# Optimization experiments

Measured on AMD Instinct MI355X. Metric: run time of the kernel, lower is better.

Reference implementation:

```python
import jax, jax.numpy as jnp
import numpy as np

LN_EPS = 1e-5
H_STEP = 0.1


def _mm(W, x):
    # conv1d with kernel size 1 == channel matmul: [O,C] x [B,C,N] -> [B,O,N]
    return jnp.einsum('oc,bcn->bon', W, x)


def _layer_norm_all(x):
    # F.layer_norm(x, x.shape): normalize over the ENTIRE tensor, no affine
    m = jnp.mean(x)
    v = jnp.mean((x - m) ** 2)
    return (x - m) * jax.lax.rsqrt(v + LN_EPS)


def double_layer(x, K1, K2):
    # dropout omitted (eval mode / deterministic reference)
    x = _mm(K1, x)
    x = _layer_norm_all(x)
    x = jax.nn.relu(x)
    return _mm(K2, x)


def setup_inputs() -> dict:
    key = jax.random.key(0)
    ks = jax.random.split(key, 16)
    B, XIN, EIN, HID, OUT, NL = 1, 32, 32, 128, 64, 4
    N, E = 50000, 500000
    stdv = 0.001
    inp = {
        'xn': jax.random.normal(ks[0], (B, XIN, N), dtype=jnp.float32),
        'xe': jax.random.normal(ks[1], (B, EIN, E), dtype=jnp.float32),
        'iInd': jax.random.randint(ks[2], (E,), 0, N),
        'jInd': jax.random.randint(ks[3], (E,), 0, N),
        'K1Nopen': jax.random.normal(ks[4], (HID, XIN), dtype=jnp.float32) * stdv,
        'K2Nopen': jax.random.normal(ks[5], (HID, HID), dtype=jnp.float32) * stdv,
        'K1Eopen': jax.random.normal(ks[6], (HID, EIN), dtype=jnp.float32) * stdv,
        'K2Eopen': jax.random.normal(ks[7], (HID, HID), dtype=jnp.float32) * stdv,
        'KNout': jax.random.normal(ks[8], (OUT, HID), dtype=jnp.float32) * stdv,
        'KE1': jax.random.normal(ks[9], (NL, 2 * HID, 3 * HID), dtype=jnp.float32) * stdv,
        'KE2': jax.random.normal(ks[10], (NL, HID, 2 * HID), dtype=jnp.float32) * stdv,
        'KN1': jax.random.normal(ks[11], (NL, 2 * HID, 3 * HID), dtype=jnp.float32) * stdv,
        'KN2': jax.random.normal(ks[12], (NL, HID, 2 * HID), dtype=jnp.float32) * stdv,
    }
    return inp


def reference(xn, xe, iInd, jInd, K1Nopen, K2Nopen, K1Eopen, K2Eopen, KNout,
              KE1, KE2, KN1, KN2):
    xn = double_layer(xn, K1Nopen, K2Nopen)
    xe = double_layer(xe, K1Eopen, K2Eopen)
    N = xn.shape[2]
    # Source sets row = col = Graph.iInd (faithful replication)
    row = iInd
    col = iInd
    nlayers = KE1.shape[0]
    for i in range(nlayers):
        # gather node feats to edges, concat with edge feats: [B, 3*hid, E]
        xec = jnp.concatenate([xn[:, :, row], xn[:, :, col], xe], axis=1)
        xec = double_layer(xec, KE1[i], KE2[i])
        # scatter edge feats back to both endpoints
        zeros = jnp.zeros((xec.shape[0], xec.shape[1], N), dtype=xec.dtype)
        s_i = zeros.at[:, :, iInd].add(xec)
        s_j = zeros.at[:, :, jInd].add(xec)
        ave = 0.5 * (s_i + s_j)          # edgeAve(method='ave')
        div = s_i - s_j                   # edgeDiv
        xnc = jnp.concatenate([ave, div, xn], axis=1)
        xnc = double_layer(xnc, KN1[i], KN2[i])
        xn = xn + H_STEP * xnc
        xe = xe + H_STEP * xec
    xn = _mm(KNout, xn)
    return xn, xe
```

## Files before the change

kernel.cpp:

```cpp
#include <hip/hip_runtime.h>
#include <hip/hip_bf16.h>


typedef __hip_bfloat16 bf16;
typedef __attribute__((ext_vector_type(8))) short bf16x8;
typedef __attribute__((ext_vector_type(4))) float f32x4;

#define HSTEP 0.1f

__device__ __forceinline__ bf16  f2b(float v){ return __float2bfloat16(v); }
__device__ __forceinline__ unsigned int f2bu(float v){
    return (unsigned int)__builtin_bit_cast(unsigned short, __float2bfloat16(v));
}
__device__ __forceinline__ void store8(float* p, const float* a){
    *(float4*)p       = make_float4(a[0],a[1],a[2],a[3]);
    *((float4*)p + 1) = make_float4(a[4],a[5],a[6],a[7]);
}

__device__ __forceinline__ uint4 lnrelu_pack(uint4 r, float mean, float rstd){
    float f0 = __uint_as_float(r.x << 16), f1 = __uint_as_float(r.x & 0xffff0000u);
    float f2 = __uint_as_float(r.y << 16), f3 = __uint_as_float(r.y & 0xffff0000u);
    float f4 = __uint_as_float(r.z << 16), f5 = __uint_as_float(r.z & 0xffff0000u);
    float f6 = __uint_as_float(r.w << 16), f7 = __uint_as_float(r.w & 0xffff0000u);
    f0 = fmaxf(0.f,(f0-mean)*rstd); f1 = fmaxf(0.f,(f1-mean)*rstd);
    f2 = fmaxf(0.f,(f2-mean)*rstd); f3 = fmaxf(0.f,(f3-mean)*rstd);
    f4 = fmaxf(0.f,(f4-mean)*rstd); f5 = fmaxf(0.f,(f5-mean)*rstd);
    f6 = fmaxf(0.f,(f6-mean)*rstd); f7 = fmaxf(0.f,(f7-mean)*rstd);
    uint4 q;
    q.x = f2bu(f0) | (f2bu(f1) << 16);
    q.y = f2bu(f2) | (f2bu(f3) << 16);
    q.z = f2bu(f4) | (f2bu(f5) << 16);
    q.w = f2bu(f6) | (f2bu(f7) << 16);
    return q;
}
__device__ __forceinline__ uint4 pack8f(float4 a, float4 b){
    uint4 q;
    q.x = f2bu(a.x) | (f2bu(a.y) << 16);
    q.y = f2bu(a.z) | (f2bu(a.w) << 16);
    q.z = f2bu(b.x) | (f2bu(b.y) << 16);
    q.w = f2bu(b.z) | (f2bu(b.w) << 16);
    return q;
}

__device__ __forceinline__ void block_red2(double ls, double ls2, double* sredw,
                                           int tx, double* redp, int bid)
{
    #pragma unroll
    for (int off = 32; off; off >>= 1) {
        ls  += __shfl_down(ls,  off, 64);
        ls2 += __shfl_down(ls2, off, 64);
    }
    const int w = tx >> 6, l = tx & 63;
    if (l == 0) { sredw[2*w] = ls; sredw[2*w+1] = ls2; }
    __syncthreads();
    if (tx == 0) {
        redp[2*(size_t)bid]     = ((sredw[0]+sredw[2])+(sredw[4]+sredw[6]));
        redp[2*(size_t)bid + 1] = ((sredw[1]+sredw[3])+(sredw[5]+sredw[7]));
    }
}

__global__ void wt_transpose(const float* __restrict__ src, float* __restrict__ dst,
                             int O, int C) {
    int i = blockIdx.x*256 + threadIdx.x;
    if (i >= O*C) return;
    int o = i / C, c = i - o*C;
    dst[c*O + o] = src[i];
}

__global__ void wt_ke1_bf(const float* __restrict__ src, bf16* __restrict__ dst) {
    int i = blockIdx.x*256 + threadIdx.x;
    if (i >= 256*256) return;
    int o = i >> 8, c = i & 255;
    float v;
    if (c < 128) v = src[o*384 + c] + src[o*384 + 128 + c];
    else         v = src[o*384 + 128 + c];
    dst[i] = f2b(v);
}

__global__ void wt_cast_bf(const float* __restrict__ src, bf16* __restrict__ dst, int cnt) {
    int i = blockIdx.x*256 + threadIdx.x;
    if (i < cnt) dst[i] = f2b(src[i]);
}

__global__ void csr_hist(const int* __restrict__ ind, int* __restrict__ cnt, int E){
    int e = blockIdx.x*256 + threadIdx.x;
    if (e < E) atomicAdd(&cnt[ind[e]], 1);
}

__global__ void csr_scan(const int* __restrict__ cnt, int* __restrict__ rowptr,
                         int* __restrict__ cursor, int Nn)
{
    __shared__ int part[256];
    int tx = threadIdx.x;
    int chunk = (Nn + 255) / 256;
    int a0 = tx * chunk;
    int a1 = a0 + chunk; if (a1 > Nn) a1 = Nn; if (a0 > Nn) a0 = Nn;
    int s = 0;
    for (int i = a0; i < a1; ++i) s += cnt[i];
    part[tx] = s;
    __syncthreads();
    for (int d = 1; d < 256; d <<= 1) {
        int v = (tx >= d) ? part[tx - d] : 0;
        __syncthreads();
        part[tx] += v;
        __syncthreads();
    }
    int run = (tx == 0) ? 0 : part[tx - 1];
    for (int i = a0; i < a1; ++i) {
        rowptr[i] = run; cursor[i] = run;
        run += cnt[i];
    }
    if (tx == 255) rowptr[Nn] = run;
}

__global__ void csr_fill(const int* __restrict__ ind, int* __restrict__ cursor,
                         int* __restrict__ eadj, int E){
    int e = blockIdx.x*256 + threadIdx.x;
    if (e < E) {
        int p = atomicAdd(&cursor[ind[e]], 1);
        eadj[p] = e;
    }
}

__launch_bounds__(256)
__global__ void gather_nodes(const bf16* __restrict__ y,
                             const int* __restrict__ rowptr,
                             const int* __restrict__ eadj,
                             float* __restrict__ s, int Nn)
{
    int wid  = threadIdx.x >> 6;
    int lane = threadIdx.x & 63;
    int node = blockIdx.x * 4 + wid;
    if (node >= Nn) return;
    int k0 = rowptr[node], k1 = rowptr[node+1];
    const unsigned* yu = (const unsigned*)y;
    float a0=0.f,a1=0.f,b0=0.f,b1=0.f,c0=0.f,c1=0.f,d0=0.f,d1=0.f;
    int k = k0;
    for (; k + 4 <= k1; k += 4) {
        int e0 = eadj[k], e1 = eadj[k+1], e2 = eadj[k+2], e3 = eadj[k+3];
        unsigned v0 = yu[(size_t)e0*64 + lane];
        unsigned v1 = yu[(size_t)e1*64 + lane];
        unsigned v2 = yu[(size_t)e2*64 + lane];
        unsigned v3 = yu[(size_t)e3*64 + lane];
        a0 += __uint_as_float(v0 << 16); a1 += __uint_as_float(v0 & 0xffff0000u);
        b0 += __uint_as_float(v1 << 16); b1 += __uint_as_float(v1 & 0xffff0000u);
        c0 += __uint_as_float(v2 << 16); c1 += __uint_as_float(v2 & 0xffff0000u);
        d0 += __uint_as_float(v3 << 16); d1 += __uint_as_float(v3 & 0xffff0000u);
    }
    for (; k < k1; ++k) {
        unsigned v = yu[(size_t)eadj[k]*64 + lane];
        a0 += __uint_as_float(v << 16); a1 += __uint_as_float(v & 0xffff0000u);
    }
    a0 += (b0 + c0) + d0;
    a1 += (b1 + c1) + d1;
    *(float2*)(s + (size_t)node*128 + lane*2) = make_float2(a0, a1);
}

__global__ void ln_reduce(const double* __restrict__ redp, int nb,
                          float* __restrict__ ln, double cnt)
{
    __shared__ double s0[256], s1[256];
    int tx = threadIdx.x;
    double a = 0.0, b = 0.0;
    for (int i = tx; i < nb; i += 256) { a += redp[2*i]; b += redp[2*i+1]; }
    s0[tx] = a; s1[tx] = b;
    __syncthreads();
    for (int s = 128; s > 0; s >>= 1) {
        if (tx < s) { s0[tx] += s0[tx+s]; s1[tx] += s1[tx+s]; }
        __syncthreads();
    }
    if (tx == 0) {
        double m = s0[0] / cnt;
        double var = s1[0] / cnt - m*m;
        if (var < 0.0) var = 0.0;
        ln[0] = (float)m;
        ln[1] = (float)(1.0 / sqrt(var + 1e-5));
    }
}

__launch_bounds__(256)
__global__ void mfma_mm1_edge(const bf16* __restrict__ Wb,
                              const bf16* __restrict__ xnb,
                              const float* __restrict__ xe,
                              const int* __restrict__ iInd,
                              bf16* __restrict__ ucm,
                              int E, double* __restrict__ redp)
{
    __shared__ __align__(16) unsigned short Vs[64*256];
    __shared__ double sredw[8];
    const int tx = threadIdx.x;
    const int x0 = blockIdx.x * 64;
    const int e = tx >> 2, q4 = tx & 3;
    const int xedge = x0 + e;
    const bool ev = xedge < E;
    const int gidx = ev ? iInd[xedge] : 0;
    const unsigned swz = (unsigned)((e & 7) << 3);

    #pragma unroll
    for (int p = 0; p < 4; ++p) {
        int k0 = q4*8 + p*32;
        uint4 v = make_uint4(0,0,0,0);
        if (ev) v = *(const uint4*)(xnb + (size_t)gidx*128 + k0);
        *(uint4*)&Vs[(unsigned)(e*256 + k0) ^ swz] = v;
    }
    #pragma unroll
    for (int p = 0; p < 4; ++p) {
        int k0 = q4*8 + p*32;
        uint4 v = make_uint4(0,0,0,0);
        if (ev) {
            const float* s = xe + (size_t)xedge*128 + k0;
            v = pack8f(*(const float4*)s, *(const float4*)(s + 4));
        }
        *(uint4*)&Vs[(unsigned)(e*256 + 128 + k0) ^ swz] = v;
    }
    __syncthreads();

    const int w = tx >> 6, l = tx & 63;
    const int colb = l & 15, grp = l >> 4;
    f32x4 acc[4][4];
    #pragma unroll
    for (int m=0;m<4;++m)
        #pragma unroll
        for (int n=0;n<4;++n) acc[m][n] = (f32x4){0.f,0.f,0.f,0.f};

    const bf16* wp = Wb + (size_t)(w*64 + colb)*256 + grp*8;
    bf16x8 aC[4], aN[4];
    #pragma unroll
    for (int m=0;m<4;++m)
        aC[m] = __builtin_bit_cast(bf16x8, *(const uint4*)(wp + m*16*256));

    #pragma unroll
    for (int kc = 0; kc < 8; ++kc) {
        const int kf = kc*32 + grp*8;
        if (kc < 7) {
            #pragma unroll
            for (int m=0;m<4;++m)
                aN[m] = __builtin_bit_cast(bf16x8,
                          *(const uint4*)(wp + m*16*256 + (kc+1)*32));
        }
        bf16x8 b[4];
        #pragma unroll
        for (int n=0;n<4;++n) {
            int ee = n*16 + colb;
            b[n] = __builtin_bit_cast(bf16x8,
                     *(const uint4*)&Vs[(unsigned)(ee*256 + kf) ^ (unsigned)((ee&7)<<3)]);
        }
        #pragma unroll
        for (int m=0;m<4;++m)
            #pragma unroll
            for (int n=0;n<4;++n)
                acc[m][n] = __builtin_amdgcn_mfma_f32_16x16x32_bf16(aC[m], b[n], acc[m][n], 0, 0, 0);
        #pragma unroll
        for (int m=0;m<4;++m) aC[m] = aN[m];
    }

    double ls = 0.0, ls2 = 0.0;
    #pragma unroll
    for (int n=0;n<4;++n) {
        int edge = x0 + n*16 + colb;
        if (edge < E) {
            #pragma unroll
            for (int m=0;m<4;++m) {
                f32x4 v = acc[m][n];
                ls  += (double)v[0] + (double)v[1] + (double)v[2] + (double)v[3];
                ls2 += (double)v[0]*v[0] + (double)v[1]*v[1]
                     + (double)v[2]*v[2] + (double)v[3]*v[3];
            }
        }
    }

    __syncthreads();
    const int rq = grp*4;
    #pragma unroll
    for (int n=0;n<4;++n) {
        int ee = n*16 + colb;
        #pragma unroll
        for (int m=0;m<4;++m) {
            f32x4 v = acc[m][n];
            int r0 = w*64 + m*16 + rq;
            uint2 q;
            q.x = f2bu(v[0]) | (f2bu(v[1]) << 16);
            q.y = f2bu(v[2]) | (f2bu(v[3]) << 16);
            *(uint2*)&Vs[(unsigned)(ee*256 + r0) ^ (unsigned)((ee&7)<<3)] = q;
        }
    }
    __syncthreads();
    if (ev) {
        #pragma unroll
        for (int p = 0; p < 8; ++p) {
            int c0 = q4*8 + p*32;
            uint4 v = *(uint4*)&Vs[(unsigned)(e*256 + c0) ^ swz];
            *(uint4*)(ucm + (size_t)xedge*256 + c0) = v;
        }
    }
    block_red2(ls, ls2, sredw, tx, redp, blockIdx.x);
}

__launch_bounds__(256)
__global__ void mfma_mm1_node(const bf16* __restrict__ Wb,
                              const float* __restrict__ si,
                              const float* __restrict__ sj,
                              const float* __restrict__ xn,
                              bf16* __restrict__ ucm,
                              int Nn, double* __restrict__ redp)
{
    __shared__ __align__(16) unsigned short Vs[64*384];
    __shared__ double sredw[8];
    const int tx = threadIdx.x;
    const int x0 = blockIdx.x * 64;
    const int e = tx >> 2, q4 = tx & 3;
    const int node = x0 + e;
    const bool nv = node < Nn;
    const unsigned swz = (unsigned)((e & 7) << 3);

    #pragma unroll
    for (int p = 0; p < 4; ++p) {
        int k0 = q4*8 + p*32;
        uint4 va = make_uint4(0,0,0,0), vd = va;
        if (nv) {
            const float* ps = si + (size_t)node*128 + k0;
            const float* pt = sj + (size_t)node*128 + k0;
            float4 a0 = *(const float4*)ps, a1 = *(const float4*)(ps+4);
            float4 b0 = *(const float4*)pt, b1 = *(const float4*)(pt+4);
            float4 av0 = make_float4(0.5f*(a0.x+b0.x),0.5f*(a0.y+b0.y),
                                     0.5f*(a0.z+b0.z),0.5f*(a0.w+b0.w));
            float4 av1 = make_float4(0.5f*(a1.x+b1.x),0.5f*(a1.y+b1.y),
                                     0.5f*(a1.z+b1.z),0.5f*(a1.w+b1.w));
            float4 dv0 = make_float4(a0.x-b0.x,a0.y-b0.y,a0.z-b0.z,a0.w-b0.w);
            float4 dv1 = make_float4(a1.x-b1.x,a1.y-b1.y,a1.z-b1.z,a1.w-b1.w);
            va = pack8f(av0, av1);
            vd = pack8f(dv0, dv1);
        }
        *(uint4*)&Vs[(unsigned)(e*384 + k0) ^ swz] = va;
        *(uint4*)&Vs[(unsigned)(e*384 + 128 + k0) ^ swz] = vd;
    }
    #pragma unroll
    for (int p = 0; p < 4; ++p) {
        int k0 = q4*8 + p*32;
        uint4 v = make_uint4(0,0,0,0);
        if (nv) {
            const float* s = xn + (size_t)node*128 + k0;
            v = pack8f(*(const float4*)s, *(const float4*)(s + 4));
        }
        *(uint4*)&Vs[(unsigned)(e*384 + 256 + k0) ^ swz] = v;
    }
    __syncthreads();

    const int w = tx >> 6, l = tx & 63;
    const int colb = l & 15, grp = l >> 4;
    f32x4 acc[4][4];
    #pragma unroll
    for (int m=0;m<4;++m)
        #pragma unroll
        for (int n=0;n<4;++n) acc[m][n] = (f32x4){0.f,0.f,0.f,0.f};

    const bf16* wp = Wb + (size_t)(w*64 + colb)*384 + grp*8;
    bf16x8 aC[4], aN[4];
    #pragma unroll
    for (int m=0;m<4;++m)
        aC[m] = __builtin_bit_cast(bf16x8, *(const uint4*)(wp + m*16*384));

    #pragma unroll
    for (int kc = 0; kc < 12; ++kc) {
        const int kf = kc*32 + grp*8;
        if (kc < 11) {
            #pragma unroll
            for (int m=0;m<4;++m)
                aN[m] = __builtin_bit_cast(bf16x8,
                          *(const uint4*)(wp + m*16*384 + (kc+1)*32));
        }
        bf16x8 b[4];
        #pragma unroll
        for (int n=0;n<4;++n) {
            int ee = n*16 + colb;
            b[n] = __builtin_bit_cast(bf16x8,
                     *(const uint4*)&Vs[(unsigned)(ee*384 + kf) ^ (unsigned)((ee&7)<<3)]);
        }
        #pragma unroll
        for (int m=0;m<4;++m)
            #pragma unroll
            for (int n=0;n<4;++n)
                acc[m][n] = __builtin_amdgcn_mfma_f32_16x16x32_bf16(aC[m], b[n], acc[m][n], 0, 0, 0);
        #pragma unroll
        for (int m=0;m<4;++m) aC[m] = aN[m];
    }

    double ls = 0.0, ls2 = 0.0;
    const int rq = grp*4;
    #pragma unroll
    for (int n=0;n<4;++n) {
        int nd = x0 + n*16 + colb;
        if (nd < Nn) {
            #pragma unroll
            for (int m=0;m<4;++m) {
                f32x4 v = acc[m][n];
                int r0 = w*64 + m*16 + rq;
                uint2 q;
                q.x = f2bu(v[0]) | (f2bu(v[1]) << 16);
                q.y = f2bu(v[2]) | (f2bu(v[3]) << 16);
                *(uint2*)(ucm + (size_t)nd*256 + r0) = q;
                ls  += (double)v[0] + (double)v[1] + (double)v[2] + (double)v[3];
                ls2 += (double)v[0]*v[0] + (double)v[1]*v[1]
                     + (double)v[2]*v[2] + (double)v[3]*v[3];
            }
        }
    }
    block_red2(ls, ls2, sredw, tx, redp, blockIdx.x);
}

enum { E2_EDGE = 0, E2_NODE = 1, E2_XE0 = 2, E2_XN0 = 3 };

template<int IC, int EPI>
__launch_bounds__(256)
__global__ void mfma_mm2(const bf16* __restrict__ Wb2,
                         const bf16* __restrict__ ucm,
                         const float* __restrict__ ln,
                         float* __restrict__ dst,
                         bf16* __restrict__ yv,
                         bf16* __restrict__ xnb,
                         int n)
{
    __shared__ __align__(16) unsigned short Vs[64*IC];
    const int tx = threadIdx.x;
    const int x0 = blockIdx.x * 64;
    const int e = tx >> 2, q4 = tx & 3;
    const int row = x0 + e;
    const bool rv = row < n;
    const float mean = ln[0], rstd = ln[1];
    const unsigned swz = (unsigned)((e & 7) << 3);

    #pragma unroll
    for (int p = 0; p < IC/32; ++p) {
        int k0 = q4*8 + p*32;
        uint4 v = make_uint4(0,0,0,0);
        if (rv) {
            uint4 r = *(const uint4*)(ucm + (size_t)row*IC + k0);
            v = lnrelu_pack(r, mean, rstd);
        }
        *(uint4*)&Vs[(unsigned)(e*IC + k0) ^ swz] = v;
    }
    __syncthreads();

    const int w = tx >> 6, l = tx & 63;
    const int colb = l & 15, grp = l >> 4;
    f32x4 acc[2][4];
    #pragma unroll
    for (int m=0;m<2;++m)
        #pragma unroll
        for (int nn=0;nn<4;++nn) acc[m][nn] = (f32x4){0.f,0.f,0.f,0.f};

    const bf16* wp = Wb2 + (size_t)(w*32 + colb)*IC + grp*8;
    bf16x8 aC[2], aN[2];
    #pragma unroll
    for (int m=0;m<2;++m)
        aC[m] = __builtin_bit_cast(bf16x8, *(const uint4*)(wp + m*16*IC));

    #pragma unroll
    for (int kc = 0; kc < IC/32; ++kc) {
        const int kf = kc*32 + grp*8;
        if (kc < IC/32 - 1) {
            #pragma unroll
            for (int m=0;m<2;++m)
                aN[m] = __builtin_bit_cast(bf16x8,
                          *(const uint4*)(wp + m*16*IC + (kc+1)*32));
        }
        bf16x8 b[4];
        #pragma unroll
        for (int nn=0;nn<4;++nn) {
            int ee = nn*16 + colb;
            b[nn] = __builtin_bit_cast(bf16x8,
                     *(const uint4*)&Vs[(unsigned)(ee*IC + kf) ^ (unsigned)((ee&7)<<3)]);
        }
        #pragma unroll
        for (int m=0;m<2;++m)
            #pragma unroll
            for (int nn=0;nn<4;++nn)
                acc[m][nn] = __builtin_amdgcn_mfma_f32_16x16x32_bf16(aC[m], b[nn], acc[m][nn], 0, 0, 0);
        #pragma unroll
        for (int m=0;m<2;++m) aC[m] = aN[m];
    }

    const int rq = grp*4;
    #pragma unroll
    for (int nn=0;nn<4;++nn) {
        int x = x0 + nn*16 + colb;
        if (x < n) {
            #pragma unroll
            for (int m=0;m<2;++m) {
                f32x4 v = acc[m][nn];
                int r0 = w*32 + m*16 + rq;
                if constexpr (EPI == E2_EDGE) {
                    uint2 q;
                    q.x = f2bu(v[0]) | (f2bu(v[1]) << 16);
                    q.y = f2bu(v[2]) | (f2bu(v[3]) << 16);
                    *(uint2*)(yv + (size_t)x*128 + r0) = q;
                    float* px = dst + (size_t)x*128 + r0;
                    float4 o = *(float4*)px;
                    o.x += HSTEP*v[0]; o.y += HSTEP*v[1];
                    o.z += HSTEP*v[2]; o.w += HSTEP*v[3];
                    *(float4*)px = o;
                } else if constexpr (EPI == E2_XE0) {
                    *(float4*)(dst + (size_t)x*128 + r0) =
                        make_float4(v[0], v[1], v[2], v[3]);
                } else if constexpr (EPI == E2_NODE) {
                    float* px = dst + (size_t)x*128 + r0;
                    float4 o = *(float4*)px;
                    o.x += HSTEP*v[0]; o.y += HSTEP*v[1];
                    o.z += HSTEP*v[2]; o.w += HSTEP*v[3];
                    *(float4*)px = o;
                    uint2 q;
                    q.x = f2bu(o.x) | (f2bu(o.y) << 16);
                    q.y = f2bu(o.z) | (f2bu(o.w) << 16);
                    *(uint2*)(xnb + (size_t)x*128 + r0) = q;
                } else {
                    *(float4*)(dst + (size_t)x*128 + r0) =
                        make_float4(v[0], v[1], v[2], v[3]);
                    uint2 q;
                    q.x = f2bu(v[0]) | (f2bu(v[1]) << 16);
                    q.y = f2bu(v[2]) | (f2bu(v[3]) << 16);
                    *(uint2*)(xnb + (size_t)x*128 + r0) = q;
                }
            }
        }
    }
}

__launch_bounds__(256)
__global__ void mm1_open(const float* __restrict__ Wt,
                         const float* __restrict__ xin,
                         bf16* __restrict__ ucm,
                         int n, double* __restrict__ redp)
{
    __shared__ float lv[32][64];
    __shared__ double sredw[8];
    const int tx = threadIdx.x;
    const int tr = tx & 31, tc = tx >> 5;
    const int x0 = blockIdx.x * 64;

    float acc[4][8];
    #pragma unroll
    for (int ri=0; ri<4; ++ri)
        #pragma unroll
        for (int ei=0; ei<8; ++ei) acc[ri][ei] = 0.f;

    #pragma unroll
    for (int k=0; k<2; ++k) {
        int id = k*256 + tx;
        int xq = id & 15, cc = id >> 4;
        int x = x0 + xq*4;
        const float* p = xin + (size_t)cc*n + x;
        float4 q;
        if (x + 3 < n) q = *(const float4*)p;
        else {
            q.x = (x  <n)?p[0]:0.f; q.y = (x+1<n)?p[1]:0.f;
            q.z = (x+2<n)?p[2]:0.f; q.w = (x+3<n)?p[3]:0.f;
        }
        *(float4*)&lv[cc][xq*4] = q;
    }
    __syncthreads();
    for (int cc=0; cc<32; ++cc) {
        const float* wrow = Wt + cc*128 + tr*4;
        float w[4] = {wrow[0], wrow[1], wrow[2], wrow[3]};
        float vv[8];
        #pragma unroll
        for (int ei=0; ei<8; ++ei) vv[ei] = lv[cc][tc*8+ei];
        #pragma unroll
        for (int ri=0; ri<4; ++ri)
            #pragma unroll
            for (int ei=0; ei<8; ++ei)
                acc[ri][ei] = fmaf(w[ri], vv[ei], acc[ri][ei]);
    }

    double ls = 0.0, ls2 = 0.0;
    #pragma unroll
    for (int ei=0; ei<8; ++ei) {
        int x = x0 + tc*8 + ei;
        if (x < n) {
            uint2 bq;
            bq.x = f2bu(acc[0][ei]) | (f2bu(acc[1][ei]) << 16);
            bq.y = f2bu(acc[2][ei]) | (f2bu(acc[3][ei]) << 16);
            *(uint2*)(ucm + (size_t)x*128 + tr*4) = bq;
            #pragma unroll
            for (int ri=0; ri<4; ++ri) {
                double y = acc[ri][ei]; ls += y; ls2 += y*y;
            }
        }
    }
    block_red2(ls, ls2, sredw, tx, redp, blockIdx.x);
}

__launch_bounds__(256)
__global__ void final_out(const float* __restrict__ Wt,
                          const float* __restrict__ xncm,
                          float* __restrict__ out, int n)
{
    __shared__ float lv[32][64];
    const int tx = threadIdx.x;
    const int tr = tx & 31, tc = tx >> 5;
    const int x0 = blockIdx.x * 64;

    float acc[2][8];
    #pragma unroll
    for (int ri=0; ri<2; ++ri)
        #pragma unroll
        for (int ei=0; ei<8; ++ei) acc[ri][ei] = 0.f;

    for (int c0 = 0; c0 < 128; c0 += 32) {
        #pragma unroll
        for (int k=0; k<2; ++k) {
            int id = k*256 + tx;
            int xx = id & 63, cg = id >> 6;
            int x = x0 + xx;
            float4 q;
            if (x < n) q = *(const float4*)(xncm + (size_t)x*128 + c0 + cg*4);
            else { q.x=q.y=q.z=q.w=0.f; }
            lv[cg*4+0][xx]=q.x; lv[cg*4+1][xx]=q.y;
            lv[cg*4+2][xx]=q.z; lv[cg*4+3][xx]=q.w;
        }
        __syncthreads();
        for (int cc=0; cc<32; ++cc) {
            const float* wrow = Wt + (c0+cc)*64 + tr*2;
            float w0 = wrow[0], w1 = wrow[1];
            float vv[8];
            #pragma unroll
            for (int ei=0; ei<8; ++ei) vv[ei] = lv[cc][tc*8+ei];
            #pragma unroll
            for (int ei=0; ei<8; ++ei) {
                acc[0][ei] = fmaf(w0, vv[ei], acc[0][ei]);
                acc[1][ei] = fmaf(w1, vv[ei], acc[1][ei]);
            }
        }
        __syncthreads();
    }

    const bool full = (x0 + 64 <= n);
    #pragma unroll
    for (int ri=0; ri<2; ++ri) {
        int r = tr*2 + ri;
        if (full) {
            store8(out + (size_t)r*n + x0 + tc*8, acc[ri]);
        } else {
            #pragma unroll
            for (int ei=0; ei<8; ++ei) {
                int x = x0 + tc*8 + ei;
                if (x < n) out[(size_t)r*n + x] = acc[ri][ei];
            }
        }
    }
}

__launch_bounds__(256)
__global__ void xe_transpose(const float* __restrict__ xe, float* __restrict__ out, int E)
{
    __shared__ float T[128][65];
    const int tx = threadIdx.x;
    const int x0 = blockIdx.x * 64;
    const int es = tx & 63, cg = tx >> 6;
    #pragma unroll
    for (int p = 0; p < 8; ++p) {
        int c = cg*4 + p*16;
        if (x0 + es < E) {
            float4 v = *(const float4*)(xe + (size_t)(x0+es)*128 + c);
            T[c+0][es] = v.x; T[c+1][es] = v.y; T[c+2][es] = v.z; T[c+3][es] = v.w;
        }
    }
    __syncthreads();
    const int c2 = tx >> 1, eo = (tx & 1)*32;
    if (x0 + 64 <= E) {
        #pragma unroll
        for (int q = 0; q < 8; ++q) {
            float4 v = make_float4(T[c2][eo+q*4], T[c2][eo+q*4+1],
                                   T[c2][eo+q*4+2], T[c2][eo+q*4+3]);
            *(float4*)(out + (size_t)c2*E + x0 + eo + q*4) = v;
        }
    } else {
        for (int q = 0; q < 32; ++q) {
            int x = x0 + eo + q;
            if (x < E) out[(size_t)c2*E + x] = T[c2][eo+q];
        }
    }
}

extern "C" void kernel_launch(void* const* d_in, const int* in_sizes, int n_in,
                              void* d_out, int out_size, void* d_ws, size_t ws_size,
                              hipStream_t stream)
{
    const int N = in_sizes[0] / 32;
    const int E = in_sizes[1] / 32;
    const int NL = in_sizes[9] / (256*384);

    const float* xn_in = (const float*)d_in[0];
    const float* xe_in = (const float*)d_in[1];
    const int*   iInd  = (const int*)d_in[2];
    const int*   jInd  = (const int*)d_in[3];
    const float* K1N = (const float*)d_in[4];
    const float* K2N = (const float*)d_in[5];
    const float* K1E = (const float*)d_in[6];
    const float* K2E = (const float*)d_in[7];
    const float* KNo = (const float*)d_in[8];
    const float* KE1 = (const float*)d_in[9];
    const float* KE2 = (const float*)d_in[10];
    const float* KN1 = (const float*)d_in[11];
    const float* KN2 = (const float*)d_in[12];

    char* base = (char*)d_ws;
    size_t off = 0;
    auto carve = [&](size_t bytes)->void* {
        void* p = base + off; off += (bytes + 255) & ~(size_t)255; return p;
    };
    float* xn  = (float*)carve((size_t)128*N*sizeof(float));
    float* xe  = (float*)carve((size_t)128*E*sizeof(float));
    bf16*  u   = (bf16*) carve((size_t)256*E*sizeof(bf16));
    bf16*  y   = (bf16*) carve((size_t)128*E*sizeof(bf16));
    float* si  = (float*)carve((size_t)128*N*sizeof(float));
    float* sj  = (float*)carve((size_t)128*N*sizeof(float));
    float* wtsf= (float*)carve((32*128*2 + 128*64)*sizeof(float));
    bf16*  Wb   = (bf16*)carve((size_t)256*256*sizeof(bf16));
    bf16*  Wb2  = (bf16*)carve((size_t)128*256*sizeof(bf16));
    bf16*  Wn1b = (bf16*)carve((size_t)256*384*sizeof(bf16));
    bf16*  Wn2b = (bf16*)carve((size_t)128*256*sizeof(bf16));
    bf16*  K2Nb = (bf16*)carve((size_t)128*128*sizeof(bf16));
    bf16*  K2Eb = (bf16*)carve((size_t)128*128*sizeof(bf16));
    bf16*  xnb  = (bf16*)carve((size_t)128*N*sizeof(bf16));
    double* redp = (double*)carve(2*8192*sizeof(double));
    float* lnp = (float*)carve(256);
    int* cnt      = (int*)carve((size_t)N*sizeof(int));
    int* rowptr_i = (int*)carve((size_t)(N+1)*sizeof(int));
    int* rowptr_j = (int*)carve((size_t)(N+1)*sizeof(int));
    int* cur_i    = (int*)carve((size_t)N*sizeof(int));
    int* cur_j    = (int*)carve((size_t)N*sizeof(int));
    int* eadj_i   = (int*)carve((size_t)E*sizeof(int));
    int* eadj_j   = (int*)carve((size_t)E*sizeof(int));

    if (ws_size < off) return;

    float* K1Nt = wtsf;
    float* K1Et = K1Nt + 32*128;
    float* KNoT = K1Et + 32*128;

    wt_transpose<<<dim3((128*32 +255)/256),dim3(256),0,stream>>>(K1N, K1Nt, 128, 32);
    wt_transpose<<<dim3((128*32 +255)/256),dim3(256),0,stream>>>(K1E, K1Et, 128, 32);
    wt_transpose<<<dim3((64*128 +255)/256),dim3(256),0,stream>>>(KNo, KNoT, 64, 128);
    wt_cast_bf<<<dim3(64),dim3(256),0,stream>>>(K2N, K2Nb, 128*128);
    wt_cast_bf<<<dim3(64),dim3(256),0,stream>>>(K2E, K2Eb, 128*128);

    const int gN = (N + 63)/64, gE = (E + 63)/64;
    const int gEb = (E + 255)/256;

    (void)hipMemsetAsync(cnt, 0, (size_t)N*sizeof(int), stream);
    csr_hist<<<gEb,256,0,stream>>>(iInd, cnt, E);
    csr_scan<<<1,256,0,stream>>>(cnt, rowptr_i, cur_i, N);
    csr_fill<<<gEb,256,0,stream>>>(iInd, cur_i, eadj_i, E);
    (void)hipMemsetAsync(cnt, 0, (size_t)N*sizeof(int), stream);
    csr_hist<<<gEb,256,0,stream>>>(jInd, cnt, E);
    csr_scan<<<1,256,0,stream>>>(cnt, rowptr_j, cur_j, N);
    csr_fill<<<gEb,256,0,stream>>>(jInd, cur_j, eadj_j, E);

    mm1_open<<<gN,256,0,stream>>>(K1Nt, xn_in, u, N, redp);
    ln_reduce<<<1,256,0,stream>>>(redp, gN, lnp, 128.0*N);
    mfma_mm2<128,E2_XN0><<<gN,256,0,stream>>>(K2Nb, u, lnp, xn, nullptr, xnb, N);

    mm1_open<<<gE,256,0,stream>>>(K1Et, xe_in, u, E, redp);
    ln_reduce<<<1,256,0,stream>>>(redp, gE, lnp, 128.0*E);
    mfma_mm2<128,E2_XE0><<<gE,256,0,stream>>>(K2Eb, u, lnp, xe, nullptr, nullptr, E);

    for (int l = 0; l < NL; ++l) {
        wt_ke1_bf<<<dim3(256),dim3(256),0,stream>>>(KE1 + (size_t)l*256*384, Wb);
        wt_cast_bf<<<dim3(128),dim3(256),0,stream>>>(KE2 + (size_t)l*128*256, Wb2, 128*256);
        wt_cast_bf<<<dim3(384),dim3(256),0,stream>>>(KN1 + (size_t)l*256*384, Wn1b, 256*384);
        wt_cast_bf<<<dim3(128),dim3(256),0,stream>>>(KN2 + (size_t)l*128*256, Wn2b, 128*256);

        mfma_mm1_edge<<<gE,256,0,stream>>>(Wb, xnb, xe, iInd, u, E, redp);
        ln_reduce<<<1,256,0,stream>>>(redp, gE, lnp, 256.0*E);
        mfma_mm2<256,E2_EDGE><<<gE,256,0,stream>>>(Wb2, u, lnp, xe, y, nullptr, E);
        gather_nodes<<<(N+3)/4,256,0,stream>>>(y, rowptr_i, eadj_i, si, N);
        gather_nodes<<<(N+3)/4,256,0,stream>>>(y, rowptr_j, eadj_j, sj, N);

        mfma_mm1_node<<<gN,256,0,stream>>>(Wn1b, si, sj, xn, u, N, redp);
        ln_reduce<<<1,256,0,stream>>>(redp, gN, lnp, 256.0*N);
        mfma_mm2<256,E2_NODE><<<gN,256,0,stream>>>(Wn2b, u, lnp, xn, nullptr, xnb, N);
    }

    final_out<<<gN,256,0,stream>>>(KNoT, xn, (float*)d_out, N);
    xe_transpose<<<gE,256,0,stream>>>(xe, (float*)d_out + (size_t)64*N, E);
}
```

Before: 3.659 ms.

## Persistent grid-stride MFMA kernels with register prefetch and bf16 edge-feature shadow

The edge mm1 and mm2 kernels become persistent, capped at 2048 blocks, and loop over 64-column tiles. Each iteration prefetches the next tile's inputs into registers while the current tile is computed. The mm2 epilogue now also writes a bf16 shadow copy of xe, so the edge mm1 reads bf16 instead of fp32 and packing on the fly. mm1_edge drops its LDS transpose and writes its output directly. The weight-fragment double buffering is replaced with plain per-k loads, which trades register pressure against exposed load latency, and the extra shadow store adds write traffic.

```diff
diff --git a/kernel.cpp b/kernel.cpp
--- a/kernel.cpp
+++ b/kernel.cpp
@@ -181,116 +181,97 @@
 __launch_bounds__(256)
 __global__ void mfma_mm1_edge(const bf16* __restrict__ Wb,
                               const bf16* __restrict__ xnb,
-                              const float* __restrict__ xe,
+                              const bf16* __restrict__ xeb,
                               const int* __restrict__ iInd,
                               bf16* __restrict__ ucm,
-                              int E, double* __restrict__ redp)
+                              int E, int ntiles, double* __restrict__ redp)
 {
     __shared__ __align__(16) unsigned short Vs[64*256];
     __shared__ double sredw[8];
     const int tx = threadIdx.x;
-    const int x0 = blockIdx.x * 64;
     const int e = tx >> 2, q4 = tx & 3;
-    const int xedge = x0 + e;
-    const bool ev = xedge < E;
-    const int gidx = ev ? iInd[xedge] : 0;
     const unsigned swz = (unsigned)((e & 7) << 3);
-
-    #pragma unroll
-    for (int p = 0; p < 4; ++p) {
-        int k0 = q4*8 + p*32;
-        uint4 v = make_uint4(0,0,0,0);
-        if (ev) v = *(const uint4*)(xnb + (size_t)gidx*128 + k0);
-        *(uint4*)&Vs[(unsigned)(e*256 + k0) ^ swz] = v;
-    }
-    #pragma unroll
-    for (int p = 0; p < 4; ++p) {
-        int k0 = q4*8 + p*32;
-        uint4 v = make_uint4(0,0,0,0);
-        if (ev) {
-            const float* s = xe + (size_t)xedge*128 + k0;
-            v = pack8f(*(const float4*)s, *(const float4*)(s + 4));
-        }
-        *(uint4*)&Vs[(unsigned)(e*256 + 128 + k0) ^ swz] = v;
-    }
-    __syncthreads();
-
     const int w = tx >> 6, l = tx & 63;
     const int colb = l & 15, grp = l >> 4;
-    f32x4 acc[4][4];
-    #pragma unroll
-    for (int m=0;m<4;++m)
-        #pragma unroll
-        for (int n=0;n<4;++n) acc[m][n] = (f32x4){0.f,0.f,0.f,0.f};
-
-    const bf16* wp = Wb + (size_t)(w*64 + colb)*256 + grp*8;
-    bf16x8 aC[4], aN[4];
-    #pragma unroll
-    for (int m=0;m<4;++m)
-        aC[m] = __builtin_bit_cast(bf16x8, *(const uint4*)(wp + m*16*256));
-
-    #pragma unroll
-    for (int kc = 0; kc < 8; ++kc) {
-        const int kf = kc*32 + grp*8;
-        if (kc < 7) {
+
+    uint4 rN[4] = {{0,0,0,0},{0,0,0,0},{0,0,0,0},{0,0,0,0}};
+    uint4 rE[4] = {{0,0,0,0},{0,0,0,0},{0,0,0,0},{0,0,0,0}};
+
+    auto issue = [&](int tt){
+        int xedge = tt*64 + e;
+        if (xedge < E) {
+            int gidx = iInd[xedge];
+            #pragma unroll
+            for (int p=0;p<4;++p)
+                rN[p] = *(const uint4*)(xnb + (size_t)gidx*128 + q4*8 + p*32);
+            #pragma unroll
+            for (int p=0;p<4;++p)
+                rE[p] = *(const uint4*)(xeb + (size_t)xedge*128 + q4*8 + p*32);
+        }
+    };
+
+    int t = blockIdx.x;
+    if (t < ntiles) issue(t);
+    double ls = 0.0, ls2 = 0.0;
+
+    for (; t < ntiles; t += gridDim.x) {
+        #pragma unroll
+        for (int p=0;p<4;++p) {
+            int k0 = q4*8 + p*32;
+            *(uint4*)&Vs[(unsigned)(e*256 + k0) ^ swz] = rN[p];
+            *(uint4*)&Vs[(unsigned)(e*256 + 128 + k0) ^ swz] = rE[p];
+        }
+        int tn = t + gridDim.x;
+        if (tn < ntiles) issue(tn);
+        __syncthreads();
+
+        f32x4 acc[4][4];
+        #pragma unroll
+        for (int m=0;m<4;++m)
+            #pragma unroll
+            for (int n=0;n<4;++n) acc[m][n] = (f32x4){0.f,0.f,0.f,0.f};
+
+        #pragma unroll
+        for (int kc = 0; kc < 8; ++kc) {
+            const int kf = kc*32 + grp*8;
+            bf16x8 a[4], b[4];
+            #pragma unroll
+            for (int m=0;m<4;++m) {
+                int row = w*64 + m*16 + colb;
+                a[m] = __builtin_bit_cast(bf16x8, *(const uint4*)(Wb + (size_t)row*256 + kf));
+            }
+            #pragma unroll
+            for (int n=0;n<4;++n) {
+                int ee = n*16 + colb;
+                b[n] = __builtin_bit_cast(bf16x8,
+                         *(const uint4*)&Vs[(unsigned)(ee*256 + kf) ^ (unsigned)((ee&7)<<3)]);
+            }
             #pragma unroll
             for (int m=0;m<4;++m)
-                aN[m] = __builtin_bit_cast(bf16x8,
-                          *(const uint4*)(wp + m*16*256 + (kc+1)*32));
-        }
-        bf16x8 b[4];
+                #pragma unroll
+                for (int n=0;n<4;++n)
+                    acc[m][n] = __builtin_amdgcn_mfma_f32_16x16x32_bf16(a[m], b[n], acc[m][n], 0, 0, 0);
+        }
+        __syncthreads();
+
+        const int x0 = t*64, rq = grp*4;
         #pragma unroll
         for (int n=0;n<4;++n) {
-            int ee = n*16 + colb;
-            b[n] = __builtin_bit_cast(bf16x8,
-                     *(const uint4*)&Vs[(unsigned)(ee*256 + kf) ^ (unsigned)((ee&7)<<3)]);
-        }
-        #pragma unroll
-        for (int m=0;m<4;++m)
-            #pragma unroll
-            for (int n=0;n<4;++n)
-                acc[m][n] = __builtin_amdgcn_mfma_f32_16x16x32_bf16(aC[m], b[n], acc[m][n], 0, 0, 0);
-        #pragma unroll
-        for (int m=0;m<4;++m) aC[m] = aN[m];
-    }
-
-    double ls = 0.0, ls2 = 0.0;
-    #pragma unroll
-    for (int n=0;n<4;++n) {
-        int edge = x0 + n*16 + colb;
-        if (edge < E) {
-            #pragma unroll
-            for (int m=0;m<4;++m) {
-                f32x4 v = acc[m][n];
-                ls  += (double)v[0] + (double)v[1] + (double)v[2] + (double)v[3];
-                ls2 += (double)v[0]*v[0] + (double)v[1]*v[1]
-                     + (double)v[2]*v[2] + (double)v[3]*v[3];
-            }
-        }
-    }
-
-    __syncthreads();
-    const int rq = grp*4;
-    #pragma unroll
-    for (int n=0;n<4;++n) {
-        int ee = n*16 + colb;
-        #pragma unroll
-        for (int m=0;m<4;++m) {
-            f32x4 v = acc[m][n];
-            int r0 = w*64 + m*16 + rq;
-            uint2 q;
-            q.x = f2bu(v[0]) | (f2bu(v[1]) << 16);
-            q.y = f2bu(v[2]) | (f2bu(v[3]) << 16);
-            *(uint2*)&Vs[(unsigned)(ee*256 + r0) ^ (unsigned)((ee&7)<<3)] = q;
-        }
-    }
-    __syncthreads();
-    if (ev) {
-        #pragma unroll
-        for (int p = 0; p < 8; ++p) {
-            int c0 = q4*8 + p*32;
-            uint4 v = *(uint4*)&Vs[(unsigned)(e*256 + c0) ^ swz];
-            *(uint4*)(ucm + (size_t)xedge*256 + c0) = v;
+            int edge = x0 + n*16 + colb;
+            if (edge < E) {
+                #pragma unroll
+                for (int m=0;m<4;++m) {
+                    f32x4 v = acc[m][n];
+                    int r0 = w*64 + m*16 + rq;
+                    uint2 q;
+                    q.x = f2bu(v[0]) | (f2bu(v[1]) << 16);
+                    q.y = f2bu(v[2]) | (f2bu(v[3]) << 16);
+                    *(uint2*)(ucm + (size_t)edge*256 + r0) = q;
+                    ls  += (double)v[0] + (double)v[1] + (double)v[2] + (double)v[3];
+                    ls2 += (double)v[0]*v[0] + (double)v[1]*v[1]
+                         + (double)v[2]*v[2] + (double)v[3]*v[3];
+                }
+            }
         }
     }
     block_red2(ls, ls2, sredw, tx, redp, blockIdx.x);
@@ -355,21 +336,13 @@
         for (int n=0;n<4;++n) acc[m][n] = (f32x4){0.f,0.f,0.f,0.f};
 
     const bf16* wp = Wb + (size_t)(w*64 + colb)*384 + grp*8;
-    bf16x8 aC[4], aN[4];
-    #pragma unroll
-    for (int m=0;m<4;++m)
-        aC[m] = __builtin_bit_cast(bf16x8, *(const uint4*)(wp + m*16*384));
-
     #pragma unroll
     for (int kc = 0; kc < 12; ++kc) {
         const int kf = kc*32 + grp*8;
-        if (kc < 11) {
-            #pragma unroll
-            for (int m=0;m<4;++m)
-                aN[m] = __builtin_bit_cast(bf16x8,
-                          *(const uint4*)(wp + m*16*384 + (kc+1)*32));
-        }
-        bf16x8 b[4];
+        bf16x8 a[4], b[4];
+        #pragma unroll
+        for (int m=0;m<4;++m)
+            a[m] = __builtin_bit_cast(bf16x8, *(const uint4*)(wp + m*16*384 + kc*32));
         #pragma unroll
         for (int n=0;n<4;++n) {
             int ee = n*16 + colb;
@@ -380,9 +353,7 @@
         for (int m=0;m<4;++m)
             #pragma unroll
             for (int n=0;n<4;++n)
-                acc[m][n] = __builtin_amdgcn_mfma_f32_16x16x32_bf16(aC[m], b[n], acc[m][n], 0, 0, 0);
-        #pragma unroll
-        for (int m=0;m<4;++m) aC[m] = aN[m];
+                acc[m][n] = __builtin_amdgcn_mfma_f32_16x16x32_bf16(a[m], b[n], acc[m][n], 0, 0, 0);
     }
 
     double ls = 0.0, ls2 = 0.0;
@@ -417,108 +388,120 @@
                          const float* __restrict__ ln,
                          float* __restrict__ dst,
                          bf16* __restrict__ yv,
-                         bf16* __restrict__ xnb,
-                         int n)
+                         bf16* __restrict__ shadow,
+                         int n, int ntiles)
 {
     __shared__ __align__(16) unsigned short Vs[64*IC];
     const int tx = threadIdx.x;
-    const int x0 = blockIdx.x * 64;
     const int e = tx >> 2, q4 = tx & 3;
-    const int row = x0 + e;
-    const bool rv = row < n;
-    const float mean = ln[0], rstd = ln[1];
     const unsigned swz = (unsigned)((e & 7) << 3);
-
-    #pragma unroll
-    for (int p = 0; p < IC/32; ++p) {
-        int k0 = q4*8 + p*32;
-        uint4 v = make_uint4(0,0,0,0);
-        if (rv) {
-            uint4 r = *(const uint4*)(ucm + (size_t)row*IC + k0);
-            v = lnrelu_pack(r, mean, rstd);
-        }
-        *(uint4*)&Vs[(unsigned)(e*IC + k0) ^ swz] = v;
-    }
-    __syncthreads();
-
     const int w = tx >> 6, l = tx & 63;
     const int colb = l & 15, grp = l >> 4;
-    f32x4 acc[2][4];
-    #pragma unroll
-    for (int m=0;m<2;++m)
-        #pragma unroll
-        for (int nn=0;nn<4;++nn) acc[m][nn] = (f32x4){0.f,0.f,0.f,0.f};
-
-    const bf16* wp = Wb2 + (size_t)(w*32 + colb)*IC + grp*8;
-    bf16x8 aC[2], aN[2];
-    #pragma unroll
-    for (int m=0;m<2;++m)
-        aC[m] = __builtin_bit_cast(bf16x8, *(const uint4*)(wp + m*16*IC));
-
-    #pragma unroll
-    for (int kc = 0; kc < IC/32; ++kc) {
-        const int kf = kc*32 + grp*8;
-        if (kc < IC/32 - 1) {
+    const float mean = ln[0], rstd = ln[1];
+
+    uint4 ru[IC/32];
+    #pragma unroll
+    for (int p=0;p<IC/32;++p) ru[p] = make_uint4(0,0,0,0);
+
+    auto issue = [&](int tt){
+        int row = tt*64 + e;
+        if (row < n) {
+            #pragma unroll
+            for (int p=0;p<IC/32;++p)
+                ru[p] = *(const uint4*)(ucm + (size_t)row*IC + q4*8 + p*32);
+        }
+    };
+
+    int t = blockIdx.x;
+    if (t < ntiles) issue(t);
+
+    for (; t < ntiles; t += gridDim.x) {
+        #pragma unroll
+        for (int p=0;p<IC/32;++p) {
+            int k0 = q4*8 + p*32;
+            *(uint4*)&Vs[(unsigned)(e*IC + k0) ^ swz] = lnrelu_pack(ru[p], mean, rstd);
+        }
+        int tn = t + gridDim.x;
+        if (tn < ntiles) issue(tn);
+        __syncthreads();
+
+        f32x4 acc[2][4];
+        #pragma unroll
+        for (int m=0;m<2;++m)
+            #pragma unroll
+            for (int nn=0;nn<4;++nn) acc[m][nn] = (f32x4){0.f,0.f,0.f,0.f};
+
+        #pragma unroll
+        for (int kc = 0; kc < IC/32; ++kc) {
+            const int kf = kc*32 + grp*8;
+            bf16x8 a[2], b[4];
+            #pragma unroll
+            for (int m=0;m<2;++m) {
+                int rr = w*32 + m*16 + colb;
+                a[m] = __builtin_bit_cast(bf16x8, *(const uint4*)(Wb2 + (size_t)rr*IC + kf));
+            }
+            #pragma unroll
+            for (int nn=0;nn<4;++nn) {
+                int ee = nn*16 + colb;
+                b[nn] = __builtin_bit_cast(bf16x8,
+                         *(const uint4*)&Vs[(unsigned)(ee*IC + kf) ^ (unsigned)((ee&7)<<3)]);
+            }
             #pragma unroll
             for (int m=0;m<2;++m)
-                aN[m] = __builtin_bit_cast(bf16x8,
-                          *(const uint4*)(wp + m*16*IC + (kc+1)*32));
-        }
-        bf16x8 b[4];
+                #pragma unroll
+                for (int nn=0;nn<4;++nn)
+                    acc[m][nn] = __builtin_amdgcn_mfma_f32_16x16x32_bf16(a[m], b[nn], acc[m][nn], 0, 0, 0);
+        }
+        __syncthreads();
+
+        const int x0 = t*64, rq = grp*4;
         #pragma unroll
         for (int nn=0;nn<4;++nn) {
-            int ee = nn*16 + colb;
-            b[nn] = __builtin_bit_cast(bf16x8,
-                     *(const uint4*)&Vs[(unsigned)(ee*IC + kf) ^ (unsigned)((ee&7)<<3)]);
-        }
-        #pragma unroll
-        for (int m=0;m<2;++m)
-            #pragma unroll
-            for (int nn=0;nn<4;++nn)
-                acc[m][nn] = __builtin_amdgcn_mfma_f32_16x16x32_bf16(aC[m], b[nn], acc[m][nn], 0, 0, 0);
-        #pragma unroll
-        for (int m=0;m<2;++m) aC[m] = aN[m];
-    }
-
-    const int rq = grp*4;
-    #pragma unroll
-    for (int nn=0;nn<4;++nn) {
-        int x = x0 + nn*16 + colb;
-        if (x < n) {
-            #pragma unroll
-            for (int m=0;m<2;++m) {
-                f32x4 v = acc[m][nn];
-                int r0 = w*32 + m*16 + rq;
-                if constexpr (EPI == E2_EDGE) {
-                    uint2 q;
-                    q.x = f2bu(v[0]) | (f2bu(v[1]) << 16);
-                    q.y = f2bu(v[2]) | (f2bu(v[3]) << 16);
-                    *(uint2*)(yv + (size_t)x*128 + r0) = q;
-                    float* px = dst + (size_t)x*128 + r0;
-                    float4 o = *(float4*)px;
-                    o.x += HSTEP*v[0]; o.y += HSTEP*v[1];
-                    o.z += HSTEP*v[2]; o.w += HSTEP*v[3];
-                    *(float4*)px = o;
-                } else if constexpr (EPI == E2_XE0) {
-                    *(float4*)(dst + (size_t)x*128 + r0) =
-                        make_float4(v[0], v[1], v[2], v[3]);
-                } else if constexpr (EPI == E2_NODE) {
-                    float* px = dst + (size_t)x*128 + r0;
-                    float4 o = *(float4*)px;
-                    o.x += HSTEP*v[0]; o.y += HSTEP*v[1];
-                    o.z += HSTEP*v[2]; o.w += HSTEP*v[3];
-                    *(float4*)px = o;
-                    uint2 q;
-                    q.x = f2bu(o.x) | (f2bu(o.y) << 16);
-                    q.y = f2bu(o.z) | (f2bu(o.w) << 16);
-                    *(uint2*)(xnb + (size_t)x*128 + r0) = q;
-                } else {
-                    *(float4*)(dst + (size_t)x*128 + r0) =
-                        make_float4(v[0], v[1], v[2], v[3]);
-                    uint2 q;
-                    q.x = f2bu(v[0]) | (f2bu(v[1]) << 16);
-                    q.y = f2bu(v[2]) | (f2bu(v[3]) << 16);
-                    *(uint2*)(xnb + (size_t)x*128 + r0) = q;
+            int x = x0 + nn*16 + colb;
+            if (x < n) {
+                #pragma unroll
+                for (int m=0;m<2;++m) {
+                    f32x4 v = acc[m][nn];
+                    int r0 = w*32 + m*16 + rq;
+                    if constexpr (EPI == E2_EDGE) {
+                        uint2 q;
+                        q.x = f2bu(v[0]) | (f2bu(v[1]) << 16);
+                        q.y = f2bu(v[2]) | (f2bu(v[3]) << 16);
+                        *(uint2*)(yv + (size_t)x*128 + r0) = q;
+                        float* px = dst + (size_t)x*128 + r0;
+                        float4 o = *(float4*)px;
+                        o.x += HSTEP*v[0]; o.y += HSTEP*v[1];
+                        o.z += HSTEP*v[2]; o.w += HSTEP*v[3];
+                        *(float4*)px = o;
+                        uint2 sq;
+                        sq.x = f2bu(o.x) | (f2bu(o.y) << 16);
+                        sq.y = f2bu(o.z) | (f2bu(o.w) << 16);
+                        *(uint2*)(shadow + (size_t)x*128 + r0) = sq;
+                    } else if constexpr (EPI == E2_XE0) {
+                        *(float4*)(dst + (size_t)x*128 + r0) =
+                            make_float4(v[0], v[1], v[2], v[3]);
+                        uint2 sq;
+                        sq.x = f2bu(v[0]) | (f2bu(v[1]) << 16);
+                        sq.y = f2bu(v[2]) | (f2bu(v[3]) << 16);
+                        *(uint2*)(shadow + (size_t)x*128 + r0) = sq;
+                    } else if constexpr (EPI == E2_NODE) {
+                        float* px = dst + (size_t)x*128 + r0;
+                        float4 o = *(float4*)px;
+                        o.x += HSTEP*v[0]; o.y += HSTEP*v[1];
+                        o.z += HSTEP*v[2]; o.w += HSTEP*v[3];
+                        *(float4*)px = o;
+                        uint2 q;
+                        q.x = f2bu(o.x) | (f2bu(o.y) << 16);
+                        q.y = f2bu(o.z) | (f2bu(o.w) << 16);
+                        *(uint2*)(shadow + (size_t)x*128 + r0) = q;
+                    } else {
+                        *(float4*)(dst + (size_t)x*128 + r0) =
+                            make_float4(v[0], v[1], v[2], v[3]);
+                        uint2 q;
+                        q.x = f2bu(v[0]) | (f2bu(v[1]) << 16);
+                        q.y = f2bu(v[2]) | (f2bu(v[3]) << 16);
+                        *(uint2*)(shadow + (size_t)x*128 + r0) = q;
+                    }
                 }
             }
         }
@@ -710,6 +693,7 @@
     };
     float* xn  = (float*)carve((size_t)128*N*sizeof(float));
     float* xe  = (float*)carve((size_t)128*E*sizeof(float));
+    bf16*  xeb = (bf16*) carve((size_t)128*E*sizeof(bf16));
     bf16*  u   = (bf16*) carve((size_t)256*E*sizeof(bf16));
     bf16*  y   = (bf16*) carve((size_t)128*E*sizeof(bf16));
     float* si  = (float*)carve((size_t)128*N*sizeof(float));
@@ -746,6 +730,8 @@
 
     const int gN = (N + 63)/64, gE = (E + 63)/64;
     const int gEb = (E + 255)/256;
+    const int PE = (gE < 2048) ? gE : 2048;
+    const int PN = (gN < 2048) ? gN : 2048;
 
     (void)hipMemsetAsync(cnt, 0, (size_t)N*sizeof(int), stream);
     csr_hist<<<gEb,256,0,stream>>>(iInd, cnt, E);
@@ -758,11 +744,11 @@
 
     mm1_open<<<gN,256,0,stream>>>(K1Nt, xn_in, u, N, redp);
     ln_reduce<<<1,256,0,stream>>>(redp, gN, lnp, 128.0*N);
-    mfma_mm2<128,E2_XN0><<<gN,256,0,stream>>>(K2Nb, u, lnp, xn, nullptr, xnb, N);
+    mfma_mm2<128,E2_XN0><<<PN,256,0,stream>>>(K2Nb, u, lnp, xn, nullptr, xnb, N, gN);
 
     mm1_open<<<gE,256,0,stream>>>(K1Et, xe_in, u, E, redp);
     ln_reduce<<<1,256,0,stream>>>(redp, gE, lnp, 128.0*E);
-    mfma_mm2<128,E2_XE0><<<gE,256,0,stream>>>(K2Eb, u, lnp, xe, nullptr, nullptr, E);
+    mfma_mm2<128,E2_XE0><<<PE,256,0,stream>>>(K2Eb, u, lnp, xe, nullptr, xeb, E, gE);
 
     for (int l = 0; l < NL; ++l) {
         wt_ke1_bf<<<dim3(256),dim3(256),0,stream>>>(KE1 + (size_t)l*256*384, Wb);
@@ -770,15 +756,15 @@
         wt_cast_bf<<<dim3(384),dim3(256),0,stream>>>(KN1 + (size_t)l*256*384, Wn1b, 256*384);
         wt_cast_bf<<<dim3(128),dim3(256),0,stream>>>(KN2 + (size_t)l*128*256, Wn2b, 128*256);
 
-        mfma_mm1_edge<<<gE,256,0,stream>>>(Wb, xnb, xe, iInd, u, E, redp);
-        ln_reduce<<<1,256,0,stream>>>(redp, gE, lnp, 256.0*E);
-        mfma_mm2<256,E2_EDGE><<<gE,256,0,stream>>>(Wb2, u, lnp, xe, y, nullptr, E);
+        mfma_mm1_edge<<<PE,256,0,stream>>>(Wb, xnb, xeb, iInd, u, E, gE, redp);
+        ln_reduce<<<1,256,0,stream>>>(redp, PE, lnp, 256.0*E);
+        mfma_mm2<256,E2_EDGE><<<PE,256,0,stream>>>(Wb2, u, lnp, xe, y, xeb, E, gE);
         gather_nodes<<<(N+3)/4,256,0,stream>>>(y, rowptr_i, eadj_i, si, N);
         gather_nodes<<<(N+3)/4,256,0,stream>>>(y, rowptr_j, eadj_j, sj, N);
 
         mfma_mm1_node<<<gN,256,0,stream>>>(Wn1b, si, sj, xn, u, N, redp);
         ln_reduce<<<1,256,0,stream>>>(redp, gN, lnp, 256.0*N);
-        mfma_mm2<256,E2_NODE><<<gN,256,0,stream>>>(Wn2b, u, lnp, xn, nullptr, xnb, N);
+        mfma_mm2<256,E2_NODE><<<PN,256,0,stream>>>(Wn2b, u, lnp, xn, nullptr, xnb, N, gN);
     }
 
     final_out<<<gN,256,0,stream>>>(KNoT, xn, (float*)d_out, N);
```

After: 3.563 ms. -2.6%, faster.
